# Kernel optimization log

Hardware: AMD Instinct MI355X
Metric: run time of the kernel (lower is better)

The kernel has to match this reference:

```python
import jax, jax.numpy as jnp
import numpy as np

B, FEAT, Q, L, H_ENC, H_DEC = 256, 64, 16, 2, 128, 256


def _apply_1q(state, U, q):
    # state: [B, 2,2,...,2] (Q qubit axes); U: [B,2,2] complex64
    s = jnp.moveaxis(state, 1 + q, 1)
    shp = s.shape
    s2 = s.reshape(shp[0], 2, -1)
    s2 = jnp.einsum('bij,bjr->bir', U, s2)
    return jnp.moveaxis(s2.reshape(shp), 1, 1 + q)


def _apply_cnot(state, c, t):
    # flip target axis on the control=1 slice
    c0 = jnp.take(state, 0, axis=1 + c)
    c1 = jnp.take(state, 1, axis=1 + c)
    t_ax = 1 + t if t < c else t  # target axis index after removing control axis
    c1 = jnp.flip(c1, axis=t_ax)
    return jnp.stack([c0, c1], axis=1 + c)


def _u3(theta, phi, lam):
    # combined Rz(lam) @ Ry(phi) @ Rx(theta); inputs [B] -> [B,2,2] complex64
    j = jnp.complex64(1j)
    ct, st = jnp.cos(theta / 2), jnp.sin(theta / 2)
    cp, sp = jnp.cos(phi / 2), jnp.sin(phi / 2)
    Rx = jnp.stack([jnp.stack([ct + 0j, -j * st], -1),
                    jnp.stack([-j * st, ct + 0j], -1)], -2)
    Ry = jnp.stack([jnp.stack([cp + 0j, -sp + 0j], -1),
                    jnp.stack([sp + 0j, cp + 0j], -1)], -2)
    em, ep = jnp.exp(-j * lam / 2), jnp.exp(j * lam / 2)
    zero = jnp.zeros_like(em)
    Rz = jnp.stack([jnp.stack([em, zero], -1),
                    jnp.stack([zero, ep], -1)], -2)
    return jnp.einsum('bij,bjk,bkl->bil', Rz, Ry, Rx).astype(jnp.complex64)


def setup_inputs() -> dict:
    key = jax.random.key(0)
    ks = jax.random.split(key, 6)

    def xavier(k, shape):
        lim = float(np.sqrt(6.0 / (shape[0] + shape[1])))
        return jax.random.uniform(k, shape, jnp.float32, -lim, lim)

    return {
        'x': jax.random.normal(ks[0], (B, FEAT), jnp.float32),
        'W1': xavier(ks[1], (FEAT, H_ENC)), 'b1': jnp.zeros((H_ENC,), jnp.float32),
        'W2': xavier(ks[2], (H_ENC, L * Q * 3)), 'b2': jnp.zeros((L * Q * 3,), jnp.float32),
        'scaling': jnp.ones((Q,), jnp.float32),
        'Wd1': xavier(ks[3], (2 ** Q, H_DEC)), 'bd1': jnp.zeros((H_DEC,), jnp.float32),
        'Wd2': xavier(ks[4], (H_DEC, FEAT)), 'bd2': jnp.zeros((FEAT,), jnp.float32),
    }


def reference(x, W1, b1, W2, b2, scaling, Wd1, bd1, Wd2, bd2):
    batch = x.shape[0]
    nq = scaling.shape[0]
    nl = W2.shape[1] // (nq * 3)
    # classical encoder -> quantum rotation angles
    h = jax.nn.relu(x @ W1 + b1)
    p = jnp.tanh(h @ W2 + b2).reshape(batch, nl, nq, 3)
    p = p * scaling[None, None, :, None] * jnp.pi  # theta/phi/lambda scaled by pi
    # batched statevector simulation, |0...0> init
    state = jnp.zeros((batch, 2 ** nq), jnp.complex64).at[:, 0].set(1.0)
    state = state.reshape((batch,) + (2,) * nq)
    for l in range(nl):
        for q in range(nq):
            U = _u3(p[:, l, q, 0], p[:, l, q, 1], p[:, l, q, 2])
            state = _apply_1q(state, U, q)
        if l < nl - 1:
            for q in range(nq - 1):
                state = _apply_cnot(state, q, q + 1)
            state = _apply_cnot(state, nq - 1, 0)
    probs = (jnp.real(state) ** 2 + jnp.imag(state) ** 2).reshape(batch, -1)
    # classical decoder
    out = jax.nn.relu(jax.nn.relu(probs @ Wd1 + bd1) @ Wd2 + bd2)
    return out
```

## Files before the change

### kernel.cpp

```cpp
#include <hip/hip_runtime.h>
#include <hip/hip_fp16.h>

#define PI_F 3.14159265358979323846f

typedef __attribute__((ext_vector_type(8))) _Float16 f16x8;
typedef __attribute__((ext_vector_type(16))) float f32x16;
typedef __attribute__((ext_vector_type(2))) float v2f;

__device__ __forceinline__ v2f pfma(v2f a, v2f b, v2f c) {
    return __builtin_elementwise_fma(a, b, c);
}
__device__ __forceinline__ v2f vswap(v2f a) { return __builtin_shufflevector(a, a, 1, 0); }
__device__ __forceinline__ v2f vsplat(float x) { v2f r; r.x = x; r.y = x; return r; }
__device__ __forceinline__ v2f mkc(v2f u) { v2f r; r.x = -u.y; r.y = u.y; return r; }
__device__ __forceinline__ v2f cmul(v2f a, v2f b) {
    return pfma(mkc(a), vswap(b), vsplat(a.x) * b);
}

__device__ __forceinline__ unsigned f2bf_rn(float x) {
    unsigned u = __float_as_uint(x);
    return (u + 0x7fffu + ((u >> 16) & 1u)) >> 16;
}

union H8 { int4 i4; f16x8 v; };

__device__ __forceinline__ void gll16(const void* g, void* l) {
    __builtin_amdgcn_global_load_lds(
        (const __attribute__((address_space(1))) void*)g,
        (__attribute__((address_space(3))) void*)l, 16, 0, 0);
}

union EncConvLds {
    struct {
        float xr[64]; float h[128]; float ang[96];
        v2f vL[32];
        v2f uL[64];
    } e;
    _Float16 wt[64][260];
};

__global__ __launch_bounds__(256) void k_enc_chain(
        const float* __restrict__ x, const float* __restrict__ W1,
        const float* __restrict__ b1, const float* __restrict__ W2,
        const float* __restrict__ b2, const float* __restrict__ scaling,
        const float* __restrict__ Wd1, _Float16* __restrict__ Wt,
        _Float16* __restrict__ Lb, _Float16* __restrict__ Rb) {
    __shared__ EncConvLds lds;
    const int t = threadIdx.x;
    if (blockIdx.x >= 256) {
        const int cb = blockIdx.x - 256;
        const int kb = (cb >> 2) * 256;
        const int nb = (cb & 3) * 64;
        #pragma unroll
        for (int it = 0; it < 16; ++it) {
            int idx = t + it*256;
            int kr = idx >> 4;
            int nc = (idx & 15) * 4;
            float4 w = *(const float4*)(Wd1 + (size_t)(kb + kr)*256 + nb + nc);
            lds.wt[nc+0][kr] = (_Float16)(w.x * 64.f);
            lds.wt[nc+1][kr] = (_Float16)(w.y * 64.f);
            lds.wt[nc+2][kr] = (_Float16)(w.z * 64.f);
            lds.wt[nc+3][kr] = (_Float16)(w.w * 64.f);
        }
        __syncthreads();
        const int n = t >> 2, ck = t & 3;
        _Float16* dst = Wt + ((size_t)(nb + n) << 16) + kb + ck*64;
        #pragma unroll
        for (int i = 0; i < 8; ++i) {
            uint2 lo = *(const uint2*)&lds.wt[n][ck*64 + i*8];
            uint2 hi = *(const uint2*)&lds.wt[n][ck*64 + i*8 + 4];
            int4 v = make_int4((int)lo.x, (int)lo.y, (int)hi.x, (int)hi.y);
            *(int4*)(dst + i*8) = v;
        }
        return;
    }
    const int b = blockIdx.x;
    if (t < 64) lds.e.xr[t] = x[b*64 + t];
    __syncthreads();
    if (t < 128) {
        float acc = b1[t];
        #pragma unroll 8
        for (int f = 0; f < 64; ++f) acc = fmaf(lds.e.xr[f], W1[f*128 + t], acc);
        lds.e.h[t] = fmaxf(acc, 0.f);
    }
    __syncthreads();
    if (t < 96) {
        float acc = b2[t];
        #pragma unroll 8
        for (int f = 0; f < 128; ++f) acc = fmaf(lds.e.h[f], W2[f*96 + t], acc);
        int q = (t/3) & 15;
        lds.e.ang[t] = tanhf(acc) * scaling[q] * PI_F;
    }
    __syncthreads();
    if (t < 32) {
        int l = t >> 4, q = t & 15;
        const float* a = lds.e.ang + l*48 + q*3;
        float st, ct, sp, cp, sl, cl;
        sincosf(a[0]*0.5f, &st, &ct);
        sincosf(a[1]*0.5f, &sp, &cp);
        sincosf(a[2]*0.5f, &sl, &cl);
        float2 A00 = make_float2( cp*ct,  sp*st);
        float2 A01 = make_float2(-sp*ct, -cp*st);
        float2 A10 = make_float2( sp*ct, -cp*st);
        float2 A11 = make_float2( cp*ct, -sp*st);
        float2 e0 = make_float2(cl, -sl), e1 = make_float2(cl, sl);
        v2f r00; r00.x = e0.x*A00.x - e0.y*A00.y; r00.y = e0.x*A00.y + e0.y*A00.x;
        v2f r01; r01.x = e0.x*A01.x - e0.y*A01.y; r01.y = e0.x*A01.y + e0.y*A01.x;
        v2f r10; r10.x = e1.x*A10.x - e1.y*A10.y; r10.y = e1.x*A10.y + e1.y*A10.x;
        v2f r11; r11.x = e1.x*A11.x - e1.y*A11.y; r11.y = e1.x*A11.y + e1.y*A11.x;
        if (l == 0) {
            lds.e.vL[q*2 + 0] = r00;
            lds.e.vL[q*2 + 1] = r10;
        } else {
            lds.e.uL[q*4 + 0] = r00; lds.e.uL[q*4 + 1] = r01;
            lds.e.uL[q*4 + 2] = r10; lds.e.uL[q*4 + 3] = r11;
        }
    }
    __syncthreads();
    #define AP(p, s) lds.e.vL[(15-(p))*2 + (s)]
    #define GG(p, zv, yv) lds.e.uL[(15-(p))*4 + (zv)*2 + (yv)]
    const float SL = 32.f;
    v2f Lg[2][2];
    {
        int z0 = t & 1, z1 = (t >> 1) & 1;
        #pragma unroll
        for (int g = 0; g < 2; ++g)
            #pragma unroll
            for (int y = 0; y < 2; ++y)
                Lg[g][y] = cmul(cmul(GG(0, z0, g), AP(0, g ^ y)), GG(1, z1, y));
        #pragma unroll
        for (int p = 2; p <= 7; ++p) {
            int zp = (t >> p) & 1;
            #pragma unroll
            for (int g = 0; g < 2; ++g) {
                v2f s0 = cmul(Lg[g][0], AP(p-1, 0)) + cmul(Lg[g][1], AP(p-1, 1));
                v2f s1 = cmul(Lg[g][0], AP(p-1, 1)) + cmul(Lg[g][1], AP(p-1, 0));
                Lg[g][0] = cmul(s0, GG(p, zp, 0));
                Lg[g][1] = cmul(s1, GG(p, zp, 1));
            }
        }
    }
    v2f Rg[2][2];
    {
        int z15 = (t >> 7) & 1;
        #pragma unroll
        for (int g = 0; g < 2; ++g)
            #pragma unroll
            for (int y14 = 0; y14 < 2; ++y14)
                Rg[g][y14] = cmul(cmul(AP(14, y14 ^ g),     AP(15, g)),     GG(15, z15, 0))
                           + cmul(cmul(AP(14, y14 ^ 1 ^ g), AP(15, 1 ^ g)), GG(15, z15, 1));
        #pragma unroll
        for (int p = 14; p >= 8; --p) {
            int zp = (t >> (p - 8)) & 1;
            #pragma unroll
            for (int g = 0; g < 2; ++g) {
                v2f t0 = cmul(GG(p, zp, 0), Rg[g][0]);
                v2f t1 = cmul(GG(p, zp, 1), Rg[g][1]);
                v2f n0 = cmul(AP(p-1, 0), t0) + cmul(AP(p-1, 1), t1);
                v2f n1 = cmul(AP(p-1, 1), t0) + cmul(AP(p-1, 0), t1);
                Rg[g][0] = n0; Rg[g][1] = n1;
            }
        }
    }
    float lre[4] = {Lg[0][0].x, Lg[0][1].x, Lg[1][0].x, Lg[1][1].x};
    float lim[4] = {Lg[0][0].y, Lg[0][1].y, Lg[1][0].y, Lg[1][1].y};
    float rre[4] = {Rg[0][0].x, Rg[0][1].x, Rg[1][0].x, Rg[1][1].x};
    float rim[4] = {Rg[0][0].y, Rg[0][1].y, Rg[1][0].y, Rg[1][1].y};
    H8 hre, him, hr;
    #pragma unroll
    for (int k = 0; k < 4; ++k) {
        hre.v[k]   = (_Float16)(SL * lre[k]);
        hre.v[4+k] = (_Float16)(-SL * lim[k]);
        him.v[k]   = (_Float16)(SL * lim[k]);
        him.v[4+k] = (_Float16)(SL * lre[k]);
        hr.v[k]    = (_Float16)(SL * rre[k]);
        hr.v[4+k]  = (_Float16)(SL * rim[k]);
    }
    *(int4*)(Lb + ((size_t)b*512 + t)*8)       = hre.i4;
    *(int4*)(Lb + ((size_t)b*512 + 256 + t)*8) = him.i4;
    *(int4*)(Rb + ((size_t)b*256 + t)*8)       = hr.i4;
    #undef AP
    #undef GG
}

__global__ __launch_bounds__(256) void k_amp(
        const _Float16* __restrict__ Lb, const _Float16* __restrict__ Rb,
        _Float16* __restrict__ A) {
    __shared__ _Float16 lR[256*8];
    __shared__ _Float16 lL[512*8];
    const int b = blockIdx.x, t = threadIdx.x;
    {
        const float4* gl = (const float4*)(Lb + (size_t)b*512*8);
        float4* sl = (float4*)lL;
        sl[t] = gl[t];
        sl[t+256] = gl[t+256];
        ((float4*)lR)[t] = ((const float4*)(Rb + (size_t)b*256*8))[t];
    }
    __syncthreads();
    const int wave = t >> 6, lane = t & 63, h = lane >> 5, l32 = lane & 31;
    f16x8 zf = {};
    _Float16* Aout = A + ((size_t)b << 16);
    #pragma unroll
    for (int mt2 = 0; mt2 < 2; ++mt2) {
        const int zh0 = (wave*2 + mt2)*32;
        f16x8 af = h ? zf : *(const f16x8*)&lR[(zh0 + l32)*8];
        #pragma unroll
        for (int j = 0; j < 8; ++j) {
            f16x8 bre = h ? zf : *(const f16x8*)&lL[(j*32 + l32)*8];
            f16x8 bim = h ? zf : *(const f16x8*)&lL[(256 + j*32 + l32)*8];
            f32x16 zc = {};
            f32x16 dre = __builtin_amdgcn_mfma_f32_32x32x16_f16(af, bre, zc, 0, 0, 0);
            f32x16 dim = __builtin_amdgcn_mfma_f32_32x32x16_f16(af, bim, zc, 0, 0, 0);
            #pragma unroll
            for (int q = 0; q < 16; ++q) {
                float p = fmaf(dre[q], dre[q], dim[q]*dim[q]) * 0.00390625f;
                int row = zh0 + 4*h + (q & 3) + 8*(q >> 2);
                Aout[row*256 + j*32 + l32] = (_Float16)p;
            }
        }
    }
}

__global__ __launch_bounds__(256, 4) void k_gemm(
        const _Float16* __restrict__ A, const _Float16* __restrict__ Bt,
        unsigned short* __restrict__ partial) {
    __shared__ _Float16 lA[128*64];
    __shared__ _Float16 lB[128*64];
    const int ks = blockIdx.x, nt = blockIdx.y, mt = blockIdx.z;
    const int k0 = ks*256, n0 = nt*128, m0 = mt*128;
    const int tid = threadIdx.x, wave = tid >> 6, lane = tid & 63;
    const int mw = wave >> 1, nw = wave & 1;
    const int h = lane >> 5, l32 = lane & 31;
    f32x16 acc[2][2] = {};
    for (int s = 0; s < 4; ++s) {
        const int kb = k0 + s*64;
        #pragma unroll
        for (int i = 0; i < 4; ++i) {
            int ia = wave*4 + i;
            int r = ia*8 + (lane >> 3);
            int cch = (lane & 7) ^ (r & 7);
            gll16(A  + (size_t)(m0 + r)*65536 + kb + cch*8, &lA[ia*512]);
            gll16(Bt + (size_t)(n0 + r)*65536 + kb + cch*8, &lB[ia*512]);
        }
        __syncthreads();
        #pragma unroll
        for (int kk = 0; kk < 4; ++kk) {
            const int ch = kk*2 + h;
            f16x8 af[2], bf[2];
            #pragma unroll
            for (int xx = 0; xx < 2; ++xx) {
                int rA = mw*64 + xx*32 + l32;
                af[xx] = *(const f16x8*)&lA[rA*64 + ((ch ^ (rA & 7)) << 3)];
                int rB = nw*64 + xx*32 + l32;
                bf[xx] = *(const f16x8*)&lB[rB*64 + ((ch ^ (rB & 7)) << 3)];
            }
            #pragma unroll
            for (int i = 0; i < 2; ++i)
                #pragma unroll
                for (int jj = 0; jj < 2; ++jj)
                    acc[i][jj] = __builtin_amdgcn_mfma_f32_32x32x16_f16(af[i], bf[jj], acc[i][jj], 0, 0, 0);
        }
        __syncthreads();
    }
    unsigned short* pp = partial + (size_t)ks*65536;
    #pragma unroll
    for (int i = 0; i < 2; ++i) {
        #pragma unroll
        for (int jj = 0; jj < 2; ++jj) {
            int n = n0 + nw*64 + jj*32 + l32;
            int mb = m0 + mw*64 + i*32 + 4*h;
            #pragma unroll
            for (int q = 0; q < 16; ++q) {
                int m = mb + (q & 3) + 8*(q >> 2);
                pp[m*256 + n] = (unsigned short)f2bf_rn(acc[i][jj][q]);
            }
        }
    }
}

__global__ __launch_bounds__(256) void k_final(
        const unsigned short* __restrict__ partial, const float* __restrict__ bd1,
        const float* __restrict__ Wd2, const float* __restrict__ bd2,
        float* __restrict__ out) {
    __shared__ float row[256];
    const int m = blockIdx.x, t = threadIdx.x;
    if (t < 128) {
        const unsigned* p = (const unsigned*)partial + m*128 + t;
        float s0 = 0.f, s1 = 0.f;
        #pragma unroll 8
        for (int kc = 0; kc < 256; ++kc) {
            unsigned u = p[(size_t)kc*32768];
            s0 += __uint_as_float(u << 16);
            s1 += __uint_as_float(u & 0xffff0000u);
        }
        const float SC = 1.f / 262144.f;
        row[2*t]   = fmaxf(fmaf(s0, SC, bd1[2*t]),   0.f);
        row[2*t+1] = fmaxf(fmaf(s1, SC, bd1[2*t+1]), 0.f);
    }
    __syncthreads();
    if (t < 64) {
        float o = bd2[t];
        #pragma unroll 8
        for (int n = 0; n < 256; ++n) o = fmaf(row[n], Wd2[n*64 + t], o);
        out[m*64 + t] = fmaxf(o, 0.f);
    }
}

extern "C" void kernel_launch(void* const* d_in, const int* in_sizes, int n_in,
                              void* d_out, int out_size, void* d_ws, size_t ws_size,
                              hipStream_t stream) {
    const float* x       = (const float*)d_in[0];
    const float* W1      = (const float*)d_in[1];
    const float* b1      = (const float*)d_in[2];
    const float* W2      = (const float*)d_in[3];
    const float* b2      = (const float*)d_in[4];
    const float* scaling = (const float*)d_in[5];
    const float* Wd1     = (const float*)d_in[6];
    const float* bd1     = (const float*)d_in[7];
    const float* Wd2     = (const float*)d_in[8];
    const float* bd2     = (const float*)d_in[9];
    float* out = (float*)d_out;

    char* ws = (char*)d_ws;
    const size_t MB = 1024*1024;
    _Float16* Lb = (_Float16*)(ws + 0);
    _Float16* Rb = (_Float16*)(ws + 2*MB);
    _Float16* A  = (_Float16*)(ws + 4*MB);
    _Float16* Wt = (_Float16*)(ws + 36*MB);
    unsigned short* partial = (unsigned short*)(ws + 68*MB);

    hipLaunchKernelGGL(k_enc_chain, dim3(1280), dim3(256), 0, stream,
                       x, W1, b1, W2, b2, scaling, Wd1, Wt, Lb, Rb);
    hipLaunchKernelGGL(k_amp, dim3(256), dim3(256), 0, stream, Lb, Rb, A);
    hipLaunchKernelGGL(k_gemm, dim3(256, 2, 2), dim3(256), 0, stream, A, Wt, partial);
    hipLaunchKernelGGL(k_final, dim3(256), dim3(256), 0, stream,
                       partial, bd1, Wd2, bd2, out);
}
```

Baseline: 183.7 us.

## Fuse amplitude kernel into encoder chain and split partial reduction into two stages

The separate amplitude kernel is folded into the encoder/chain kernel: the L and R factors now stay in shared memory and feed the MFMA probability computation directly, so they are no longer written to and re-read from global workspace. The Wd1 transpose write-out is reorganised so each lane stores a contiguous 16-byte row chunk. The final split-K reduction over 256 bf16 partials is split into a wide 2048-block pre-reduction kernel plus a small 8-way sum in the final kernel, to spread the strided partial reads across more parallelism. This adds one kernel launch and an fp32 intermediate buffer, and the fused kernel uses more LDS.

```diff
diff --git a/kernel.cpp b/kernel.cpp
--- a/kernel.cpp
+++ b/kernel.cpp
@@ -30,22 +30,24 @@
         (__attribute__((address_space(3))) void*)l, 16, 0, 0);
 }
 
-union EncConvLds {
+union PreLds {
     struct {
         float xr[64]; float h[128]; float ang[96];
         v2f vL[32];
         v2f uL[64];
+        _Float16 lR[256*8];
+        _Float16 lL[512*8];
     } e;
     _Float16 wt[64][260];
 };
 
-__global__ __launch_bounds__(256) void k_enc_chain(
+__global__ __launch_bounds__(256) void k_pre(
         const float* __restrict__ x, const float* __restrict__ W1,
         const float* __restrict__ b1, const float* __restrict__ W2,
         const float* __restrict__ b2, const float* __restrict__ scaling,
         const float* __restrict__ Wd1, _Float16* __restrict__ Wt,
-        _Float16* __restrict__ Lb, _Float16* __restrict__ Rb) {
-    __shared__ EncConvLds lds;
+        _Float16* __restrict__ A) {
+    __shared__ PreLds lds;
     const int t = threadIdx.x;
     if (blockIdx.x >= 256) {
         const int cb = blockIdx.x - 256;
@@ -63,14 +65,13 @@
             lds.wt[nc+3][kr] = (_Float16)(w.w * 64.f);
         }
         __syncthreads();
-        const int n = t >> 2, ck = t & 3;
-        _Float16* dst = Wt + ((size_t)(nb + n) << 16) + kb + ck*64;
-        #pragma unroll
-        for (int i = 0; i < 8; ++i) {
-            uint2 lo = *(const uint2*)&lds.wt[n][ck*64 + i*8];
-            uint2 hi = *(const uint2*)&lds.wt[n][ck*64 + i*8 + 4];
-            int4 v = make_int4((int)lo.x, (int)lo.y, (int)hi.x, (int)hi.y);
-            *(int4*)(dst + i*8) = v;
+        const int wv = t >> 6, ln = t & 63;
+        const int u = ln & 31;
+        #pragma unroll
+        for (int r = 0; r < 8; ++r) {
+            int n = r*8 + wv*2 + (ln >> 5);
+            int4 hh = *(const int4*)&lds.wt[n][u*8];
+            *(int4*)(Wt + ((size_t)(nb + n) << 16) + kb + u*8) = hh;
         }
         return;
     }
@@ -162,60 +163,49 @@
             }
         }
     }
-    float lre[4] = {Lg[0][0].x, Lg[0][1].x, Lg[1][0].x, Lg[1][1].x};
-    float lim[4] = {Lg[0][0].y, Lg[0][1].y, Lg[1][0].y, Lg[1][1].y};
-    float rre[4] = {Rg[0][0].x, Rg[0][1].x, Rg[1][0].x, Rg[1][1].x};
-    float rim[4] = {Rg[0][0].y, Rg[0][1].y, Rg[1][0].y, Rg[1][1].y};
-    H8 hre, him, hr;
-    #pragma unroll
-    for (int k = 0; k < 4; ++k) {
-        hre.v[k]   = (_Float16)(SL * lre[k]);
-        hre.v[4+k] = (_Float16)(-SL * lim[k]);
-        him.v[k]   = (_Float16)(SL * lim[k]);
-        him.v[4+k] = (_Float16)(SL * lre[k]);
-        hr.v[k]    = (_Float16)(SL * rre[k]);
-        hr.v[4+k]  = (_Float16)(SL * rim[k]);
-    }
-    *(int4*)(Lb + ((size_t)b*512 + t)*8)       = hre.i4;
-    *(int4*)(Lb + ((size_t)b*512 + 256 + t)*8) = him.i4;
-    *(int4*)(Rb + ((size_t)b*256 + t)*8)       = hr.i4;
     #undef AP
     #undef GG
-}
-
-__global__ __launch_bounds__(256) void k_amp(
-        const _Float16* __restrict__ Lb, const _Float16* __restrict__ Rb,
-        _Float16* __restrict__ A) {
-    __shared__ _Float16 lR[256*8];
-    __shared__ _Float16 lL[512*8];
-    const int b = blockIdx.x, t = threadIdx.x;
-    {
-        const float4* gl = (const float4*)(Lb + (size_t)b*512*8);
-        float4* sl = (float4*)lL;
-        sl[t] = gl[t];
-        sl[t+256] = gl[t+256];
-        ((float4*)lR)[t] = ((const float4*)(Rb + (size_t)b*256*8))[t];
-    }
-    __syncthreads();
-    const int wave = t >> 6, lane = t & 63, h = lane >> 5, l32 = lane & 31;
-    f16x8 zf = {};
-    _Float16* Aout = A + ((size_t)b << 16);
-    #pragma unroll
-    for (int mt2 = 0; mt2 < 2; ++mt2) {
-        const int zh0 = (wave*2 + mt2)*32;
-        f16x8 af = h ? zf : *(const f16x8*)&lR[(zh0 + l32)*8];
-        #pragma unroll
-        for (int j = 0; j < 8; ++j) {
-            f16x8 bre = h ? zf : *(const f16x8*)&lL[(j*32 + l32)*8];
-            f16x8 bim = h ? zf : *(const f16x8*)&lL[(256 + j*32 + l32)*8];
-            f32x16 zc = {};
-            f32x16 dre = __builtin_amdgcn_mfma_f32_32x32x16_f16(af, bre, zc, 0, 0, 0);
-            f32x16 dim = __builtin_amdgcn_mfma_f32_32x32x16_f16(af, bim, zc, 0, 0, 0);
-            #pragma unroll
-            for (int q = 0; q < 16; ++q) {
-                float p = fmaf(dre[q], dre[q], dim[q]*dim[q]) * 0.00390625f;
-                int row = zh0 + 4*h + (q & 3) + 8*(q >> 2);
-                Aout[row*256 + j*32 + l32] = (_Float16)p;
+    {
+        float lre[4] = {Lg[0][0].x, Lg[0][1].x, Lg[1][0].x, Lg[1][1].x};
+        float lim[4] = {Lg[0][0].y, Lg[0][1].y, Lg[1][0].y, Lg[1][1].y};
+        float rre[4] = {Rg[0][0].x, Rg[0][1].x, Rg[1][0].x, Rg[1][1].x};
+        float rim[4] = {Rg[0][0].y, Rg[0][1].y, Rg[1][0].y, Rg[1][1].y};
+        H8 hre, him, hr;
+        #pragma unroll
+        for (int k = 0; k < 4; ++k) {
+            hre.v[k]   = (_Float16)(SL * lre[k]);
+            hre.v[4+k] = (_Float16)(-SL * lim[k]);
+            him.v[k]   = (_Float16)(SL * lim[k]);
+            him.v[4+k] = (_Float16)(SL * lre[k]);
+            hr.v[k]    = (_Float16)(SL * rre[k]);
+            hr.v[4+k]  = (_Float16)(SL * rim[k]);
+        }
+        *(int4*)&lds.e.lR[t*8]         = hr.i4;
+        *(int4*)&lds.e.lL[t*8]         = hre.i4;
+        *(int4*)&lds.e.lL[(256+t)*8]   = him.i4;
+    }
+    __syncthreads();
+    {
+        const int wave = t >> 6, lane = t & 63, h2 = lane >> 5, l32 = lane & 31;
+        f16x8 zf = {};
+        _Float16* Aout = A + ((size_t)b << 16);
+        #pragma unroll
+        for (int mt2 = 0; mt2 < 2; ++mt2) {
+            const int zh0 = (wave*2 + mt2)*32;
+            f16x8 af = h2 ? zf : *(const f16x8*)&lds.e.lR[(zh0 + l32)*8];
+            #pragma unroll
+            for (int j = 0; j < 8; ++j) {
+                f16x8 bre = h2 ? zf : *(const f16x8*)&lds.e.lL[(j*32 + l32)*8];
+                f16x8 bim = h2 ? zf : *(const f16x8*)&lds.e.lL[(256 + j*32 + l32)*8];
+                f32x16 zc = {};
+                f32x16 dre = __builtin_amdgcn_mfma_f32_32x32x16_f16(af, bre, zc, 0, 0, 0);
+                f32x16 dim = __builtin_amdgcn_mfma_f32_32x32x16_f16(af, bim, zc, 0, 0, 0);
+                #pragma unroll
+                for (int q = 0; q < 16; ++q) {
+                    float p = fmaf(dre[q], dre[q], dim[q]*dim[q]) * 0.00390625f;
+                    int row = zh0 + 4*h2 + (q & 3) + 8*(q >> 2);
+                    Aout[row*256 + j*32 + l32] = (_Float16)p;
+                }
             }
         }
     }
@@ -278,24 +268,31 @@
     }
 }
 
+__global__ __launch_bounds__(256) void k_red(
+        const unsigned short* __restrict__ partial, float* __restrict__ partial2) {
+    const int m = blockIdx.x & 255, g = blockIdx.x >> 8;
+    const int t = threadIdx.x;
+    const unsigned short* p = partial + (size_t)(g*32)*65536 + m*256 + t;
+    float s = 0.f;
+    #pragma unroll 8
+    for (int kc = 0; kc < 32; ++kc)
+        s += __uint_as_float(((unsigned)p[(size_t)kc*65536]) << 16);
+    partial2[((size_t)g*256 + m)*256 + t] = s;
+}
+
 __global__ __launch_bounds__(256) void k_final(
-        const unsigned short* __restrict__ partial, const float* __restrict__ bd1,
+        const float* __restrict__ partial2, const float* __restrict__ bd1,
         const float* __restrict__ Wd2, const float* __restrict__ bd2,
         float* __restrict__ out) {
     __shared__ float row[256];
     const int m = blockIdx.x, t = threadIdx.x;
-    if (t < 128) {
-        const unsigned* p = (const unsigned*)partial + m*128 + t;
-        float s0 = 0.f, s1 = 0.f;
-        #pragma unroll 8
-        for (int kc = 0; kc < 256; ++kc) {
-            unsigned u = p[(size_t)kc*32768];
-            s0 += __uint_as_float(u << 16);
-            s1 += __uint_as_float(u & 0xffff0000u);
-        }
+    {
+        float s = 0.f;
+        #pragma unroll
+        for (int g = 0; g < 8; ++g)
+            s += partial2[((size_t)g*256 + m)*256 + t];
         const float SC = 1.f / 262144.f;
-        row[2*t]   = fmaxf(fmaf(s0, SC, bd1[2*t]),   0.f);
-        row[2*t+1] = fmaxf(fmaf(s1, SC, bd1[2*t+1]), 0.f);
+        row[t] = fmaxf(fmaf(s, SC, bd1[t]), 0.f);
     }
     __syncthreads();
     if (t < 64) {
@@ -323,16 +320,15 @@
 
     char* ws = (char*)d_ws;
     const size_t MB = 1024*1024;
-    _Float16* Lb = (_Float16*)(ws + 0);
-    _Float16* Rb = (_Float16*)(ws + 2*MB);
     _Float16* A  = (_Float16*)(ws + 4*MB);
     _Float16* Wt = (_Float16*)(ws + 36*MB);
     unsigned short* partial = (unsigned short*)(ws + 68*MB);
-
-    hipLaunchKernelGGL(k_enc_chain, dim3(1280), dim3(256), 0, stream,
-                       x, W1, b1, W2, b2, scaling, Wd1, Wt, Lb, Rb);
-    hipLaunchKernelGGL(k_amp, dim3(256), dim3(256), 0, stream, Lb, Rb, A);
+    float* partial2 = (float*)(ws + 100*MB);
+
+    hipLaunchKernelGGL(k_pre, dim3(1280), dim3(256), 0, stream,
+                       x, W1, b1, W2, b2, scaling, Wd1, Wt, A);
     hipLaunchKernelGGL(k_gemm, dim3(256, 2, 2), dim3(256), 0, stream, A, Wt, partial);
+    hipLaunchKernelGGL(k_red, dim3(2048), dim3(256), 0, stream, partial, partial2);
     hipLaunchKernelGGL(k_final, dim3(256), dim3(256), 0, stream,
-                       partial, bd1, Wd2, bd2, out);
-}
+                       partial2, bd1, Wd2, bd2, out);
+}
```

Measured after the change: 172.4 us. 1.07x faster.
